# Performance work log

Hardware: AMD Instinct MI355X
Metric: run time of the kernel (lower is better)

The kernel has to match this reference:

```python
import jax, jax.numpy as jnp
import numpy as np

N = 50000
F_DIM = 128
H_DIM = 128
E = 800000


def setup_inputs() -> dict:
    key = jax.random.key(0)
    ks = jax.random.split(key, 8)
    x = jax.random.normal(ks[0], (N, F_DIM), dtype=jnp.float32)
    edge_weight = jax.random.uniform(ks[1], (E,), dtype=jnp.float32)
    src = jax.random.randint(ks[2], (E,), 0, N)
    dst = jax.random.randint(ks[3], (E,), 0, N)
    edge_index = jnp.stack([src, dst]).astype(jnp.int64)
    sc = 1.0 / np.sqrt(F_DIM)
    W1 = jax.random.normal(ks[4], (F_DIM, H_DIM), dtype=jnp.float32) * sc
    W2 = jax.random.normal(ks[5], (H_DIM, H_DIM), dtype=jnp.float32) * sc
    Wfc = jax.random.normal(ks[6], (H_DIM, F_DIM), dtype=jnp.float32) * sc
    b1 = jnp.zeros((H_DIM,), jnp.float32)
    b2 = jnp.zeros((H_DIM,), jnp.float32)
    bfc = jnp.zeros((F_DIM,), jnp.float32)
    return {"x": x, "edge_weight": edge_weight, "W1": W1, "b1": b1,
            "W2": W2, "b2": b2, "Wfc": Wfc, "bfc": bfc,
            "edge_index": edge_index}


def _gcn_norm(src, dst, edge_weight, num_nodes):
    # PyG gcn_norm: add self-loops (weight 1), symmetric D^-1/2 A D^-1/2
    loop = jnp.arange(num_nodes, dtype=src.dtype)
    src2 = jnp.concatenate([src, loop])
    dst2 = jnp.concatenate([dst, loop])
    w2 = jnp.concatenate([edge_weight, jnp.ones((num_nodes,), edge_weight.dtype)])
    deg = jax.ops.segment_sum(w2, dst2, num_segments=num_nodes)
    dinv = jnp.where(deg > 0, jax.lax.rsqrt(jnp.where(deg > 0, deg, 1.0)), 0.0)
    norm = dinv[src2] * w2 * dinv[dst2]
    return src2, dst2, norm


def _gcn_conv(x, W, b, src, dst, norm, num_nodes):
    h = x @ W                              # [N, out]
    msg = norm[:, None] * h[src]           # gather + scale, [E+N, out]
    agg = jax.ops.segment_sum(msg, dst, num_segments=num_nodes)
    return agg + b


def reference(x, edge_weight, W1, b1, W2, b2, Wfc, bfc, edge_index):
    src, dst = edge_index[0], edge_index[1]
    src2, dst2, norm = _gcn_norm(src, dst, edge_weight, N)
    h = jax.nn.relu(_gcn_conv(x, W1, b1, src2, dst2, norm, N))
    h = jax.nn.relu(_gcn_conv(h, W2, b2, src2, dst2, norm, N))
    return h @ Wfc + bfc
```

## Files before the change

kernel.cpp:

```cpp
#include <hip/hip_runtime.h>
#include <hip/hip_fp16.h>


typedef unsigned long long u64;
typedef _Float16 f16x8 __attribute__((ext_vector_type(8)));
typedef float f32x4 __attribute__((ext_vector_type(4)));

#define CAP 96

__global__ __launch_bounds__(256) void k_pre(unsigned* cnt, int n,
                                             const float* __restrict__ W1,
                                             const float* __restrict__ W2,
                                             const float* __restrict__ Wfc,
                                             __half* __restrict__ Wt) {
    int i = blockIdx.x * 256 + threadIdx.x;
    if (i < n) cnt[i] = 0u;
    if (i < 3 * 16384) {
        int w = i >> 14, r = i & 16383;
        int nn = r >> 7, kk = r & 127;
        const float* W = (w == 0) ? W1 : (w == 1) ? W2 : Wfc;
        Wt[i] = __float2half(W[kk * 128 + nn]);
    }
}

__global__ __launch_bounds__(256) void k_bucket(const int* __restrict__ src,
                                                const int* __restrict__ dst,
                                                const float* __restrict__ ew,
                                                unsigned* __restrict__ cnt,
                                                int2* __restrict__ slots, int E) {
    int e = blockIdx.x * 256 + threadIdx.x;
    if (e < E) {
        int d = dst[e];
        unsigned pos = atomicAdd(&cnt[d], 1u);
        if (pos < CAP)
            slots[(size_t)d * CAP + pos] = make_int2(src[e], __float_as_int(ew[e]));
    }
}

__global__ __launch_bounds__(256) void k_deg(const int2* __restrict__ slots,
                                             const unsigned* __restrict__ cnt,
                                             float* __restrict__ dinv, int n) {
    int wid = (blockIdx.x * 256 + threadIdx.x) >> 6;
    int lane = threadIdx.x & 63;
    if (wid >= n) return;
    int i = __builtin_amdgcn_readfirstlane(wid);
    int c = min((int)cnt[i], CAP);
    float w = 0.f;
    if (lane < c) w = __int_as_float(slots[(size_t)i * CAP + lane].y);
#pragma unroll
    for (int off = 32; off > 0; off >>= 1) w += __shfl_xor(w, off);
    if (lane == 0) dinv[i] = rsqrtf(1.0f + w);
}

template <bool IN_FP32, bool OUT_HALF>
__global__ __launch_bounds__(256) void k_gemm(const void* __restrict__ Xv,
                                              const __half* __restrict__ Wt,
                                              const float* __restrict__ bias,
                                              void* __restrict__ Yv, int n) {
    __shared__ __align__(16) _Float16 Ws[128][136];
    int t = threadIdx.x;
    for (int i = t; i < 2048; i += 256) {
        int r = i >> 4, c8 = (i & 15) << 3;
        *(f16x8*)&Ws[r][c8] = *(const f16x8*)((const _Float16*)Wt + r * 128 + c8);
    }
    __syncthreads();

    int wave = t >> 6, lane = t & 63;
    int quad = lane >> 4, fcol = lane & 15;
    int rowbase = blockIdx.x * 64 + wave * 16;
    int arow = rowbase + fcol;

    f16x8 a[4];
#pragma unroll
    for (int c = 0; c < 4; c++) {
        int k0 = c * 32 + quad * 8;
        if (arow < n) {
            if (IN_FP32) {
                const float* p = (const float*)Xv + (size_t)arow * 128 + k0;
#pragma unroll
                for (int j = 0; j < 8; j++) a[c][j] = (_Float16)p[j];
            } else {
                a[c] = *(const f16x8*)((const _Float16*)Xv + (size_t)arow * 128 + k0);
            }
        } else {
            f16x8 z = {0, 0, 0, 0, 0, 0, 0, 0};
            a[c] = z;
        }
    }

    f32x4 acc[8];
#pragma unroll
    for (int c = 0; c < 8; c++) acc[c] = (f32x4){0.f, 0.f, 0.f, 0.f};

#pragma unroll
    for (int kc = 0; kc < 4; kc++) {
        int k0 = kc * 32 + quad * 8;
#pragma unroll
        for (int ct = 0; ct < 8; ct++) {
            f16x8 b = *(const f16x8*)&Ws[ct * 16 + fcol][k0];
            acc[ct] = __builtin_amdgcn_mfma_f32_16x16x32_f16(a[kc], b, acc[ct], 0, 0, 0);
        }
    }

#pragma unroll
    for (int reg = 0; reg < 4; reg++) {
        int gr = rowbase + quad * 4 + reg;
        if (gr < n) {
            if (OUT_HALF) {
                __half* Y = (__half*)Yv;
#pragma unroll
                for (int ct = 0; ct < 8; ct++)
                    Y[(size_t)gr * 128 + ct * 16 + fcol] = __float2half(acc[ct][reg]);
            } else {
                float* Y = (float*)Yv;
#pragma unroll
                for (int ct = 0; ct < 8; ct++)
                    Y[(size_t)gr * 128 + ct * 16 + fcol] = acc[ct][reg] + bias[ct * 16 + fcol];
            }
        }
    }
}

__global__ __launch_bounds__(256) void k_agg(const __half* __restrict__ H,
                                             const int2* __restrict__ slots,
                                             const unsigned* __restrict__ cnt,
                                             const float* __restrict__ dinv,
                                             const float* __restrict__ bias,
                                             __half* __restrict__ out, int n) {
    int wid = (blockIdx.x * 256 + threadIdx.x) >> 6;
    int lane = threadIdx.x & 63;
    if (wid >= n) return;
    int i = __builtin_amdgcn_readfirstlane(wid);
    float di = dinv[i];
    float2 h0 = __half22float2(((const __half2*)(H + (size_t)i * 128))[lane]);
    float ax = di * di * h0.x, ay = di * di * h0.y;
    int c = min((int)cnt[i], CAP);
    const int2* row = slots + (size_t)i * CAP;

    for (int base = 0; base < c; base += 64) {
        int cnt2 = min(64, c - base);
        int mys = 0; float myv = 0.f;
        if (lane < cnt2) {
            int2 pr = row[base + lane];
            mys = pr.x;
            myv = dinv[pr.x] * __int_as_float(pr.y) * di;
        }
        int j = 0;
        for (; j + 16 <= cnt2; j += 16) {
            float2 h[16];
            float v[16];
#pragma unroll
            for (int u = 0; u < 16; u++) {
                int s = __shfl(mys, j + u);
                v[u] = __shfl(myv, j + u);
                h[u] = __half22float2(((const __half2*)(H + (size_t)s * 128))[lane]);
            }
#pragma unroll
            for (int u = 0; u < 16; u++) {
                ax = fmaf(v[u], h[u].x, ax);
                ay = fmaf(v[u], h[u].y, ay);
            }
        }
        for (; j < cnt2; j += 8) {
            float2 h[8];
            float v[8];
#pragma unroll
            for (int u = 0; u < 8; u++) {
                int idx = j + u;
                int lsrc = min(idx, cnt2 - 1);
                int s = __shfl(mys, lsrc);
                float tv = __shfl(myv, lsrc);
                v[u] = (idx < cnt2) ? tv : 0.f;
                h[u] = __half22float2(((const __half2*)(H + (size_t)s * 128))[lane]);
            }
#pragma unroll
            for (int u = 0; u < 8; u++) {
                ax = fmaf(v[u], h[u].x, ax);
                ay = fmaf(v[u], h[u].y, ay);
            }
        }
    }
    float2 b = ((const float2*)bias)[lane];
    ax = fmaxf(ax + b.x, 0.f);
    ay = fmaxf(ay + b.y, 0.f);
    ((__half2*)(out + (size_t)i * 128))[lane] = __floats2half2_rn(ax, ay);
}

extern "C" void kernel_launch(void* const* d_in, const int* in_sizes, int n_in,
                              void* d_out, int out_size, void* d_ws, size_t ws_size,
                              hipStream_t stream) {
    const float* x   = (const float*)d_in[0];
    const float* ew  = (const float*)d_in[1];
    const float* W1  = (const float*)d_in[2];
    const float* b1  = (const float*)d_in[3];
    const float* W2  = (const float*)d_in[4];
    const float* b2  = (const float*)d_in[5];
    const float* Wfc = (const float*)d_in[6];
    const float* bfc = (const float*)d_in[7];
    const int* eidx  = (const int*)d_in[8];

    const int E = in_sizes[1];
    const int N = in_sizes[0] / 128;
    const int* src = eidx;
    const int* dst = eidx + E;

    char* ws = (char*)d_ws;
    size_t off = 0;
    auto alloc = [&](size_t bytes) -> void* {
        void* p = ws + off;
        off = (off + bytes + 255) & ~(size_t)255;
        return p;
    };
    int eb = (E + 255) / 256;
    int gb = (N + 63) / 64;
    int ab = (N * 64 + 255) / 256;
    int pb = (max(N, 3 * 16384) + 255) / 256;
    int Npad = N + 64;

    unsigned* cnt  = (unsigned*)alloc((size_t)N * 4);
    float*  dinv   = (float*)alloc((size_t)N * 4);
    int2*   slots  = (int2*)alloc((size_t)N * CAP * 8);
    __half* Wt     = (__half*)alloc((size_t)3 * 16384 * 2);
    __half* bufH   = (__half*)alloc((size_t)Npad * 128 * 2);
    __half* bufA   = (__half*)alloc((size_t)Npad * 128 * 2);

    k_pre<<<pb, 256, 0, stream>>>(cnt, N, W1, W2, Wfc, Wt);
    k_bucket<<<eb, 256, 0, stream>>>(src, dst, ew, cnt, slots, E);
    k_deg<<<ab, 256, 0, stream>>>(slots, cnt, dinv, N);

    k_gemm<true, true><<<gb, 256, 0, stream>>>(x, Wt, nullptr, bufH, N);
    k_agg<<<ab, 256, 0, stream>>>(bufH, slots, cnt, dinv, b1, bufA, N);
    k_gemm<false, true><<<gb, 256, 0, stream>>>(bufA, Wt + 16384, nullptr, bufH, N);
    k_agg<<<ab, 256, 0, stream>>>(bufH, slots, cnt, dinv, b2, bufA, N);
    k_gemm<false, false><<<gb, 256, 0, stream>>>(bufA, Wt + 2 * 16384, bfc, d_out, N);
}
```

Baseline: 237.8 us.

## Fuse edge bucketing with first GEMM and split aggregation across wave pairs

Merges the edge-bucketing pass and the first dense GEMM into one launch, interleaving GEMM blocks among bucketing blocks so the two independent workloads share the GPU. The GEMM in that fused kernel reads weights straight from global memory instead of staging them in LDS. Aggregation now uses two waves per node, each handling half the neighbor list, with partial sums combined through shared memory and a block barrier. This aims to shorten per-node gather latency chains and cut launch count, at the cost of half-empty waves for low-degree nodes and extra synchronization.

```diff
diff --git a/kernel.cpp b/kernel.cpp
--- a/kernel.cpp
+++ b/kernel.cpp
@@ -23,17 +23,83 @@
     }
 }
 
-__global__ __launch_bounds__(256) void k_bucket(const int* __restrict__ src,
-                                                const int* __restrict__ dst,
-                                                const float* __restrict__ ew,
-                                                unsigned* __restrict__ cnt,
-                                                int2* __restrict__ slots, int E) {
-    int e = blockIdx.x * 256 + threadIdx.x;
-    if (e < E) {
-        int d = dst[e];
-        unsigned pos = atomicAdd(&cnt[d], 1u);
-        if (pos < CAP)
-            slots[(size_t)d * CAP + pos] = make_int2(src[e], __float_as_int(ew[e]));
+template <bool IN_FP32, bool OUT_HALF>
+__device__ __forceinline__ void gemm_body_nolds(int bid, int t,
+                                                const void* __restrict__ Xv,
+                                                const _Float16* __restrict__ Wt,
+                                                const float* __restrict__ bias,
+                                                void* __restrict__ Yv, int n) {
+    int wave = t >> 6, lane = t & 63;
+    int quad = lane >> 4, fcol = lane & 15;
+    int rowbase = bid * 64 + wave * 16;
+    int arow = rowbase + fcol;
+
+    f16x8 a[4];
+#pragma unroll
+    for (int c = 0; c < 4; c++) {
+        int k0 = c * 32 + quad * 8;
+        if (arow < n) {
+            if (IN_FP32) {
+                const float* p = (const float*)Xv + (size_t)arow * 128 + k0;
+#pragma unroll
+                for (int j = 0; j < 8; j++) a[c][j] = (_Float16)p[j];
+            } else {
+                a[c] = *(const f16x8*)((const _Float16*)Xv + (size_t)arow * 128 + k0);
+            }
+        } else {
+            f16x8 z = {0, 0, 0, 0, 0, 0, 0, 0};
+            a[c] = z;
+        }
+    }
+    f32x4 acc[8];
+#pragma unroll
+    for (int c = 0; c < 8; c++) acc[c] = (f32x4){0.f, 0.f, 0.f, 0.f};
+#pragma unroll
+    for (int kc = 0; kc < 4; kc++) {
+        int k0 = kc * 32 + quad * 8;
+#pragma unroll
+        for (int ct = 0; ct < 8; ct++) {
+            f16x8 b = *(const f16x8*)(Wt + (size_t)(ct * 16 + fcol) * 128 + k0);
+            acc[ct] = __builtin_amdgcn_mfma_f32_16x16x32_f16(a[kc], b, acc[ct], 0, 0, 0);
+        }
+    }
+#pragma unroll
+    for (int reg = 0; reg < 4; reg++) {
+        int gr = rowbase + quad * 4 + reg;
+        if (gr < n) {
+            if (OUT_HALF) {
+                __half* Y = (__half*)Yv;
+#pragma unroll
+                for (int ct = 0; ct < 8; ct++)
+                    Y[(size_t)gr * 128 + ct * 16 + fcol] = __float2half(acc[ct][reg]);
+            } else {
+                float* Y = (float*)Yv;
+#pragma unroll
+                for (int ct = 0; ct < 8; ct++)
+                    Y[(size_t)gr * 128 + ct * 16 + fcol] = acc[ct][reg] + bias[ct * 16 + fcol];
+            }
+        }
+    }
+}
+
+__global__ __launch_bounds__(256) void k_bucket_gemm1(
+        const int* __restrict__ src, const int* __restrict__ dst,
+        const float* __restrict__ ew, unsigned* __restrict__ cnt,
+        int2* __restrict__ slots, int E, int gb,
+        const float* __restrict__ x, const _Float16* __restrict__ Wt,
+        __half* __restrict__ bufH, int n) {
+    int b = blockIdx.x, t = threadIdx.x;
+    if ((b % 5 == 0) && (b / 5 < gb)) {
+        gemm_body_nolds<true, true>(b / 5, t, x, Wt, nullptr, bufH, n);
+    } else {
+        int bb = b - min(b / 5 + 1, gb);
+        int e = bb * 256 + t;
+        if (e < E) {
+            int d = dst[e];
+            unsigned pos = atomicAdd(&cnt[d], 1u);
+            if (pos < CAP)
+                slots[(size_t)d * CAP + pos] = make_int2(src[e], __float_as_int(ew[e]));
+        }
     }
 }
 
@@ -87,11 +153,9 @@
             a[c] = z;
         }
     }
-
     f32x4 acc[8];
 #pragma unroll
     for (int c = 0; c < 8; c++) acc[c] = (f32x4){0.f, 0.f, 0.f, 0.f};
-
 #pragma unroll
     for (int kc = 0; kc < 4; kc++) {
         int k0 = kc * 32 + quad * 8;
@@ -101,7 +165,6 @@
             acc[ct] = __builtin_amdgcn_mfma_f32_16x16x32_f16(a[kc], b, acc[ct], 0, 0, 0);
         }
     }
-
 #pragma unroll
     for (int reg = 0; reg < 4; reg++) {
         int gr = rowbase + quad * 4 + reg;
@@ -127,63 +190,78 @@
                                              const float* __restrict__ dinv,
                                              const float* __restrict__ bias,
                                              __half* __restrict__ out, int n) {
-    int wid = (blockIdx.x * 256 + threadIdx.x) >> 6;
-    int lane = threadIdx.x & 63;
-    if (wid >= n) return;
-    int i = __builtin_amdgcn_readfirstlane(wid);
+    __shared__ float2 part[2][64];
+    int t = threadIdx.x;
+    int lane = t & 63;
+    int waveid = t >> 6;
+    int pairid = waveid >> 1;
+    int sub = waveid & 1;
+    int node = blockIdx.x * 2 + pairid;
+    bool valid = node < n;
+    int i = __builtin_amdgcn_readfirstlane(valid ? node : (n - 1));
     float di = dinv[i];
-    float2 h0 = __half22float2(((const __half2*)(H + (size_t)i * 128))[lane]);
-    float ax = di * di * h0.x, ay = di * di * h0.y;
     int c = min((int)cnt[i], CAP);
+    int h = (c + 1) >> 1;
+    int start = sub ? h : 0;
+    int len = sub ? (c - h) : h;
     const int2* row = slots + (size_t)i * CAP;
 
-    for (int base = 0; base < c; base += 64) {
-        int cnt2 = min(64, c - base);
-        int mys = 0; float myv = 0.f;
-        if (lane < cnt2) {
-            int2 pr = row[base + lane];
-            mys = pr.x;
-            myv = dinv[pr.x] * __int_as_float(pr.y) * di;
-        }
-        int j = 0;
-        for (; j + 16 <= cnt2; j += 16) {
-            float2 h[16];
-            float v[16];
-#pragma unroll
-            for (int u = 0; u < 16; u++) {
-                int s = __shfl(mys, j + u);
-                v[u] = __shfl(myv, j + u);
-                h[u] = __half22float2(((const __half2*)(H + (size_t)s * 128))[lane]);
-            }
-#pragma unroll
-            for (int u = 0; u < 16; u++) {
-                ax = fmaf(v[u], h[u].x, ax);
-                ay = fmaf(v[u], h[u].y, ay);
-            }
-        }
-        for (; j < cnt2; j += 8) {
-            float2 h[8];
-            float v[8];
-#pragma unroll
-            for (int u = 0; u < 8; u++) {
-                int idx = j + u;
-                int lsrc = min(idx, cnt2 - 1);
-                int s = __shfl(mys, lsrc);
-                float tv = __shfl(myv, lsrc);
-                v[u] = (idx < cnt2) ? tv : 0.f;
-                h[u] = __half22float2(((const __half2*)(H + (size_t)s * 128))[lane]);
-            }
-#pragma unroll
-            for (int u = 0; u < 8; u++) {
-                ax = fmaf(v[u], h[u].x, ax);
-                ay = fmaf(v[u], h[u].y, ay);
-            }
-        }
-    }
-    float2 b = ((const float2*)bias)[lane];
-    ax = fmaxf(ax + b.x, 0.f);
-    ay = fmaxf(ay + b.y, 0.f);
-    ((__half2*)(out + (size_t)i * 128))[lane] = __floats2half2_rn(ax, ay);
+    float ax = 0.f, ay = 0.f;
+    if (!sub) {
+        float2 h0 = __half22float2(((const __half2*)(H + (size_t)i * 128))[lane]);
+        ax = di * di * h0.x;
+        ay = di * di * h0.y;
+    }
+    int mys = 0; float myv = 0.f;
+    if (lane < len) {
+        int2 pr = row[start + lane];
+        mys = pr.x;
+        myv = dinv[pr.x] * __int_as_float(pr.y) * di;
+    }
+    int j = 0;
+    for (; j + 16 <= len; j += 16) {
+        float2 hh[16];
+        float v[16];
+#pragma unroll
+        for (int u = 0; u < 16; u++) {
+            int s = __shfl(mys, j + u);
+            v[u] = __shfl(myv, j + u);
+            hh[u] = __half22float2(((const __half2*)(H + (size_t)s * 128))[lane]);
+        }
+#pragma unroll
+        for (int u = 0; u < 16; u++) {
+            ax = fmaf(v[u], hh[u].x, ax);
+            ay = fmaf(v[u], hh[u].y, ay);
+        }
+    }
+    for (; j < len; j += 8) {
+        float2 hh[8];
+        float v[8];
+#pragma unroll
+        for (int u = 0; u < 8; u++) {
+            int idx = j + u;
+            int lsrc = min(idx, len - 1);
+            int s = __shfl(mys, lsrc);
+            float tv = __shfl(myv, lsrc);
+            v[u] = (idx < len) ? tv : 0.f;
+            hh[u] = __half22float2(((const __half2*)(H + (size_t)s * 128))[lane]);
+        }
+#pragma unroll
+        for (int u = 0; u < 8; u++) {
+            ax = fmaf(v[u], hh[u].x, ax);
+            ay = fmaf(v[u], hh[u].y, ay);
+        }
+    }
+
+    if (!sub) part[pairid][lane] = make_float2(ax, ay);
+    __syncthreads();
+    if (sub && valid) {
+        float2 p = part[pairid][lane];
+        float2 b = ((const float2*)bias)[lane];
+        float rx = fmaxf(p.x + ax + b.x, 0.f);
+        float ry = fmaxf(p.y + ay + b.y, 0.f);
+        ((__half2*)(out + (size_t)i * 128))[lane] = __floats2half2_rn(rx, ry);
+    }
 }
 
 extern "C" void kernel_launch(void* const* d_in, const int* in_sizes, int n_in,
@@ -213,7 +291,8 @@
     };
     int eb = (E + 255) / 256;
     int gb = (N + 63) / 64;
-    int ab = (N * 64 + 255) / 256;
+    int db = (N * 64 + 255) / 256;
+    int ab = (N + 1) / 2;
     int pb = (max(N, 3 * 16384) + 255) / 256;
     int Npad = N + 64;
 
@@ -224,11 +303,13 @@
     __half* bufH   = (__half*)alloc((size_t)Npad * 128 * 2);
     __half* bufA   = (__half*)alloc((size_t)Npad * 128 * 2);
 
+    const _Float16* Wt1 = (const _Float16*)Wt;
+
     k_pre<<<pb, 256, 0, stream>>>(cnt, N, W1, W2, Wfc, Wt);
-    k_bucket<<<eb, 256, 0, stream>>>(src, dst, ew, cnt, slots, E);
-    k_deg<<<ab, 256, 0, stream>>>(slots, cnt, dinv, N);
-
-    k_gemm<true, true><<<gb, 256, 0, stream>>>(x, Wt, nullptr, bufH, N);
+    k_bucket_gemm1<<<eb + gb, 256, 0, stream>>>(src, dst, ew, cnt, slots, E, gb,
+                                                x, Wt1, bufH, N);
+    k_deg<<<db, 256, 0, stream>>>(slots, cnt, dinv, N);
+
     k_agg<<<ab, 256, 0, stream>>>(bufH, slots, cnt, dinv, b1, bufA, N);
     k_gemm<false, true><<<gb, 256, 0, stream>>>(bufA, Wt + 16384, nullptr, bufH, N);
     k_agg<<<ab, 256, 0, stream>>>(bufH, slots, cnt, dinv, b2, bufA, N);
```

Result: slower. 254.0 us (+6.8%).
